# Performance work log

Hardware: AMD Instinct MI355X
Metric: run time of the kernel (lower is better)

## Reference

```python
import jax, jax.numpy as jnp
import numpy as np

B, T, D = 2, 2048, 1024
E, DFF, TOPK = 8, 4096, 2
TEMPERATURE = 1.0


def setup_inputs() -> dict:
    key = jax.random.key(0)
    k_x, k_w1, k_w2, k_r = jax.random.split(key, 4)
    x = jax.random.normal(k_x, (B, T, D), dtype=jnp.float32)
    # Expert params: linear1 [d_ff, d_model], linear2 [d_model, d_ff], stacked over experts
    W1 = jax.random.normal(k_w1, (E, DFF, D), dtype=jnp.float32) * 0.02
    W2 = jax.random.normal(k_w2, (E, D, DFF), dtype=jnp.float32) * 0.02
    Wr = jax.random.normal(k_r, (E, D), dtype=jnp.float32) * 0.02  # router linear [num_experts, d_model]
    return {"x": x, "W1": W1, "W2": W2, "Wr": Wr}


def reference(x, W1, W2, Wr):
    # ---- TemperatureRouter: softmax(logits / T) -> top-k -> renormalize ----
    logits = jnp.einsum('btd,ed->bte', x, Wr)                  # [B,T,E]
    probs = jax.nn.softmax(logits / TEMPERATURE, axis=-1)
    topk_vals, topk_idx = jax.lax.top_k(probs, TOPK)           # [B,T,K]
    router_weights = topk_vals / topk_vals.sum(-1, keepdims=True)
    # Per-token combine gate over experts (top-k indices are distinct, so this
    # matches the per-expert masked gather/scatter-add of the torch loop)
    one_hot = jax.nn.one_hot(topk_idx, E, dtype=x.dtype)       # [B,T,K,E]
    gate = jnp.einsum('btk,btke->bte', router_weights, one_hot)  # [B,T,E]
    # ---- Experts: SiLU FFN (dropout=0 / eval), dense over all experts ----
    h = jax.nn.silu(jnp.einsum('btd,efd->btef', x, W1))        # [B,T,E,DFF]
    y = jnp.einsum('btef,edf->bted', h, W2)                    # [B,T,E,D]
    out = jnp.einsum('bte,bted->btd', gate, y)                 # [B,T,D]
    return out
```

## Files before the change

### kernel.cpp

```cpp
#include <hip/hip_runtime.h>
#include <hip/hip_bf16.h>
#include <stdint.h>

#define NTOK 4096
#define DMODEL 1024
#define DFF 4096
#define NE 8
#define MAXTILE 72

typedef __attribute__((ext_vector_type(8))) short short8;
typedef __attribute__((ext_vector_type(4))) float f32x4;

__device__ inline void gload_lds16(const void* g, void* l) {
  __builtin_amdgcn_global_load_lds(
      (const __attribute__((address_space(1))) unsigned int*)g,
      (__attribute__((address_space(3))) unsigned int*)l, 16, 0, 0);
}

__global__ void k_router(const float* __restrict__ x, const float* __restrict__ Wr,
                         int* __restrict__ cnt, int* __restrict__ tok_e,
                         float* __restrict__ tok_w) {
  const int lane = threadIdx.x & 63;
  const int t = blockIdx.x * 4 + (threadIdx.x >> 6);
  float acc[NE];
#pragma unroll
  for (int e = 0; e < NE; ++e) acc[e] = 0.f;
  const float* xr = x + (size_t)t * DMODEL;
  for (int c = lane; c < DMODEL; c += 64) {
    float xv = xr[c];
#pragma unroll
    for (int e = 0; e < NE; ++e) acc[e] += xv * Wr[e * DMODEL + c];
  }
#pragma unroll
  for (int e = 0; e < NE; ++e) {
#pragma unroll
    for (int off = 32; off >= 1; off >>= 1) acc[e] += __shfl_xor(acc[e], off);
  }
  if (lane == 0) {
    int e0 = 0; float m0 = acc[0];
#pragma unroll
    for (int e = 1; e < NE; ++e) if (acc[e] > m0) { m0 = acc[e]; e0 = e; }
    int e1 = -1; float m1 = -1e30f;
#pragma unroll
    for (int e = 0; e < NE; ++e) if (e != e0 && acc[e] > m1) { m1 = acc[e]; e1 = e; }
    float w0 = 1.f / (1.f + __expf(m1 - m0));
    tok_e[2 * t] = e0; tok_e[2 * t + 1] = e1;
    tok_w[2 * t] = w0; tok_w[2 * t + 1] = 1.f - w0;
    atomicAdd(&cnt[e0], 1); atomicAdd(&cnt[e1], 1);
  }
}

__global__ void k_offsets(const int* __restrict__ cnt, int* __restrict__ cursor,
                          int* __restrict__ off, int* __restrict__ meta) {
  if (threadIdx.x == 0) {
    int s = 0;
    for (int e = 0; e < NE; ++e) { off[e] = s; cursor[e] = s; s += cnt[e]; }
    off[NE] = s;
    int nt = 0;
    for (int e = 0; e < NE; ++e)
      for (int m0 = 0; m0 < cnt[e]; m0 += 128)
        meta[1 + nt++] = (e << 16) | m0;
    meta[0] = nt;
  }
}

__global__ void k_scatter(const int* __restrict__ tok_e, const float* __restrict__ tok_w,
                          int* __restrict__ cursor, int* __restrict__ pair_token,
                          float* __restrict__ pair_w) {
  const int t = blockIdx.x * blockDim.x + threadIdx.x;
  if (t >= NTOK) return;
#pragma unroll
  for (int k = 0; k < 2; ++k) {
    int e = tok_e[2 * t + k];
    int slot = atomicAdd(&cursor[e], 1);
    pair_token[slot] = t;
    pair_w[slot] = tok_w[2 * t + k];
  }
}

__global__ void k_cvt_x(const float* __restrict__ x, __hip_bfloat16* __restrict__ xb) {
  const int i = blockIdx.x * blockDim.x + threadIdx.x;
  const float4* src = (const float4*)x + (size_t)i * 2;
  float4 v0 = src[0], v1 = src[1];
  __hip_bfloat16 o8[8];
  o8[0] = __float2bfloat16(v0.x); o8[1] = __float2bfloat16(v0.y);
  o8[2] = __float2bfloat16(v0.z); o8[3] = __float2bfloat16(v0.w);
  o8[4] = __float2bfloat16(v1.x); o8[5] = __float2bfloat16(v1.y);
  o8[6] = __float2bfloat16(v1.z); o8[7] = __float2bfloat16(v1.w);
  *reinterpret_cast<float4*>(&xb[(size_t)i * 8]) = *reinterpret_cast<float4*>(o8);
}

template <int PHASE>
__global__ __launch_bounds__(256) void k_gemm(
    const __hip_bfloat16* __restrict__ A, const float* __restrict__ Bw,
    const int* __restrict__ off, const int* __restrict__ cnt,
    const int* __restrict__ meta,
    const int* __restrict__ pair_token, const float* __restrict__ pair_w,
    __hip_bfloat16* __restrict__ h, float* __restrict__ out, int BF, int fchunk) {
  if ((int)blockIdx.y >= meta[0]) return;
  const int pk = meta[1 + blockIdx.y];
  const int e = pk >> 16;
  const int m0 = pk & 0xffff;
  const int cnt_e = cnt[e];
  const int off_e = off[e];
  const int nt = blockIdx.x;

  __shared__ __align__(16) __hip_bfloat16 Alds[128 * 64];
  __shared__ __align__(16) __hip_bfloat16 Blds[128 * 64];

  const int t = threadIdx.x;
  const int lane = t & 63;
  const int w = t >> 6, wr = w >> 1, wc = w & 1;

  const int K = (PHASE == 1) ? DMODEL : BF;
  const int Astride = (PHASE == 1) ? DMODEL : BF;
  const int Bstride = (PHASE == 1) ? DMODEL : DFF;

  const __hip_bfloat16* arow[4];
  {
    int r = t >> 3;
#pragma unroll
    for (int i = 0; i < 4; ++i) {
      int gr = m0 + r + i * 32;
      if (gr > cnt_e - 1) gr = cnt_e - 1;
      int p = off_e + gr;
      size_t row = (PHASE == 1) ? (size_t)pair_token[p] : (size_t)p;
      arow[i] = A + row * Astride;
    }
  }
  const int ac = (t & 7) * 8;

  const float* Bbase = (PHASE == 1)
      ? Bw + ((size_t)e * DFF + (size_t)fchunk * BF + (size_t)nt * 128) * DMODEL
      : Bw + ((size_t)e * DMODEL + (size_t)nt * 128) * DFF + (size_t)fchunk * BF;
  const int bl16 = t & 15;
  const int brow0 = t >> 4;

  f32x4 acc[4][4];
#pragma unroll
  for (int m = 0; m < 4; ++m)
#pragma unroll
    for (int n = 0; n < 4; ++n) acc[m][n] = (f32x4){0.f, 0.f, 0.f, 0.f};

  for (int k0 = 0; k0 < K; k0 += 64) {
    __syncthreads();
#pragma unroll
    for (int i = 0; i < 4; ++i)
      gload_lds16(arow[i] + k0 + ac, &Alds[((t >> 3) + i * 32) * 64 + ac]);
#pragma unroll
    for (int s = 0; s < 8; ++s) {
      int row = s * 16 + brow0;
      const float* bp = Bbase + (size_t)row * Bstride + k0 + bl16 * 4;
      float4 v = *(const float4*)bp;
      __hip_bfloat16 q[4];
      q[0] = __float2bfloat16(v.x); q[1] = __float2bfloat16(v.y);
      q[2] = __float2bfloat16(v.z); q[3] = __float2bfloat16(v.w);
      *(ushort4*)&Blds[row * 64 + bl16 * 4] = *(ushort4*)q;
    }
    __syncthreads();
#pragma unroll
    for (int kk = 0; kk < 2; ++kk) {
      short8 af[4], bf_[4];
      const int ko = kk * 32 + (lane >> 4) * 8;
#pragma unroll
      for (int m = 0; m < 4; ++m)
        af[m] = *(const short8*)&Alds[(wr * 64 + m * 16 + (lane & 15)) * 64 + ko];
#pragma unroll
      for (int n = 0; n < 4; ++n)
        bf_[n] = *(const short8*)&Blds[(wc * 64 + n * 16 + (lane & 15)) * 64 + ko];
#pragma unroll
      for (int m = 0; m < 4; ++m)
#pragma unroll
        for (int n = 0; n < 4; ++n)
          acc[m][n] = __builtin_amdgcn_mfma_f32_16x16x32_bf16(af[m], bf_[n], acc[m][n], 0, 0, 0);
    }
  }

#pragma unroll
  for (int m = 0; m < 4; ++m) {
#pragma unroll
    for (int j = 0; j < 4; ++j) {
      const int lrow = wr * 64 + m * 16 + (lane >> 4) * 4 + j;
      const int grow = m0 + lrow;
      if (grow >= cnt_e) continue;
      const int p = off_e + grow;
      if (PHASE == 1) {
        __hip_bfloat16* hrow = h + (size_t)p * BF;
#pragma unroll
        for (int n = 0; n < 4; ++n) {
          int col = nt * 128 + wc * 64 + n * 16 + (lane & 15);
          float v = acc[m][n][j];
          v = v / (1.f + __expf(-v));
          hrow[col] = __float2bfloat16(v);
        }
      } else {
        const int tkn = pair_token[p];
        const float wgt = pair_w[p];
        float* orow = out + (size_t)tkn * DMODEL;
#pragma unroll
        for (int n = 0; n < 4; ++n) {
          int col = nt * 128 + wc * 64 + n * 16 + (lane & 15);
          atomicAdd(&orow[col], wgt * acc[m][n][j]);
        }
      }
    }
  }
}

extern "C" void kernel_launch(void* const* d_in, const int* in_sizes, int n_in,
                              void* d_out, int out_size, void* d_ws, size_t ws_size,
                              hipStream_t stream) {
  const float* x  = (const float*)d_in[0];
  const float* W1 = (const float*)d_in[1];
  const float* W2 = (const float*)d_in[2];
  const float* Wr = (const float*)d_in[3];
  float* out = (float*)d_out;

  char* ws = (char*)d_ws;
  int*   cnt        = (int*)(ws + 0);
  int*   cursor     = (int*)(ws + 256);
  int*   off        = (int*)(ws + 512);
  int*   meta       = (int*)(ws + 768);
  int*   tok_e      = (int*)(ws + 2048);
  float* tok_w      = (float*)(ws + 2048 + 32768);
  int*   pair_token = (int*)(ws + 2048 + 65536);
  float* pair_w     = (float*)(ws + 2048 + 98304);
  __hip_bfloat16* xb = (__hip_bfloat16*)(ws + 133120);
  const size_t hoff = 133120 + (size_t)NTOK * DMODEL * 2;
  __hip_bfloat16* h = (__hip_bfloat16*)(ws + hoff);

  int nchunk = 1;
  while (nchunk < 32 &&
         hoff + (unsigned long long)(2 * NTOK) * (DFF / nchunk) * 2ULL > ws_size)
    nchunk <<= 1;
  const int BF = DFF / nchunk;

  hipMemsetAsync(cnt, 0, 32, stream);
  hipMemsetAsync(d_out, 0, (size_t)out_size * sizeof(float), stream);

  k_cvt_x<<<NTOK * DMODEL / (256 * 8), 256, 0, stream>>>(x, xb);
  k_router<<<NTOK / 4, 256, 0, stream>>>(x, Wr, cnt, tok_e, tok_w);
  k_offsets<<<1, 64, 0, stream>>>(cnt, cursor, off, meta);
  k_scatter<<<NTOK / 256, 256, 0, stream>>>(tok_e, tok_w, cursor, pair_token, pair_w);

  for (int c = 0; c < nchunk; ++c) {
    k_gemm<1><<<dim3(BF / 128, MAXTILE, 1), 256, 0, stream>>>(
        xb, W1, off, cnt, meta, pair_token, pair_w, h, out, BF, c);
    k_gemm<2><<<dim3(DMODEL / 128, MAXTILE, 1), 256, 0, stream>>>(
        h, W2, off, cnt, meta, pair_token, pair_w, h, out, BF, c);
  }
}
```

Before: 704.8 us.

## Double-buffer GEMM tiles with register prefetch and fuse x conversion into router

The expert GEMM main loop now uses two LDS buffers per operand. It prefetches the next A tile via global_load_lds and the next fp32 B tile into registers while the current tile is computed, so global memory latency overlaps with the MFMA work. The separate x-to-bf16 conversion kernel is folded into the router kernel, which already reads each token row, saving one launch and one pass over x. Launch bounds request 2 blocks per SIMD, and the doubled LDS use plus 8 float4 prefetch registers may raise register pressure or limit occupancy.

```diff
diff --git a/kernel.cpp b/kernel.cpp
--- a/kernel.cpp
+++ b/kernel.cpp
@@ -19,13 +19,27 @@
 
 __global__ void k_router(const float* __restrict__ x, const float* __restrict__ Wr,
                          int* __restrict__ cnt, int* __restrict__ tok_e,
-                         float* __restrict__ tok_w) {
+                         float* __restrict__ tok_w, __hip_bfloat16* __restrict__ xb) {
   const int lane = threadIdx.x & 63;
   const int t = blockIdx.x * 4 + (threadIdx.x >> 6);
+  const float* xr = x + (size_t)t * DMODEL;
+
+  {
+    const float4* xr4 = (const float4*)xr;
+    ushort4* xb4 = (ushort4*)(xb + (size_t)t * DMODEL);
+#pragma unroll
+    for (int i = 0; i < 4; ++i) {
+      float4 v = xr4[lane + 64 * i];
+      __hip_bfloat16 q[4];
+      q[0] = __float2bfloat16(v.x); q[1] = __float2bfloat16(v.y);
+      q[2] = __float2bfloat16(v.z); q[3] = __float2bfloat16(v.w);
+      xb4[lane + 64 * i] = *(ushort4*)q;
+    }
+  }
+
   float acc[NE];
 #pragma unroll
   for (int e = 0; e < NE; ++e) acc[e] = 0.f;
-  const float* xr = x + (size_t)t * DMODEL;
   for (int c = lane; c < DMODEL; c += 64) {
     float xv = xr[c];
 #pragma unroll
@@ -78,20 +92,8 @@
   }
 }
 
-__global__ void k_cvt_x(const float* __restrict__ x, __hip_bfloat16* __restrict__ xb) {
-  const int i = blockIdx.x * blockDim.x + threadIdx.x;
-  const float4* src = (const float4*)x + (size_t)i * 2;
-  float4 v0 = src[0], v1 = src[1];
-  __hip_bfloat16 o8[8];
-  o8[0] = __float2bfloat16(v0.x); o8[1] = __float2bfloat16(v0.y);
-  o8[2] = __float2bfloat16(v0.z); o8[3] = __float2bfloat16(v0.w);
-  o8[4] = __float2bfloat16(v1.x); o8[5] = __float2bfloat16(v1.y);
-  o8[6] = __float2bfloat16(v1.z); o8[7] = __float2bfloat16(v1.w);
-  *reinterpret_cast<float4*>(&xb[(size_t)i * 8]) = *reinterpret_cast<float4*>(o8);
-}
-
 template <int PHASE>
-__global__ __launch_bounds__(256) void k_gemm(
+__global__ __launch_bounds__(256, 2) void k_gemm(
     const __hip_bfloat16* __restrict__ A, const float* __restrict__ Bw,
     const int* __restrict__ off, const int* __restrict__ cnt,
     const int* __restrict__ meta,
@@ -105,8 +107,8 @@
   const int off_e = off[e];
   const int nt = blockIdx.x;
 
-  __shared__ __align__(16) __hip_bfloat16 Alds[128 * 64];
-  __shared__ __align__(16) __hip_bfloat16 Blds[128 * 64];
+  __shared__ __align__(16) __hip_bfloat16 Alds[2][128 * 64];
+  __shared__ __align__(16) __hip_bfloat16 Blds[2][128 * 64];
 
   const int t = threadIdx.x;
   const int lane = t & 63;
@@ -115,6 +117,7 @@
   const int K = (PHASE == 1) ? DMODEL : BF;
   const int Astride = (PHASE == 1) ? DMODEL : BF;
   const int Bstride = (PHASE == 1) ? DMODEL : DFF;
+  const int NT = K >> 6;
 
   const __hip_bfloat16* arow[4];
   {
@@ -142,38 +145,55 @@
 #pragma unroll
     for (int n = 0; n < 4; ++n) acc[m][n] = (f32x4){0.f, 0.f, 0.f, 0.f};
 
-  for (int k0 = 0; k0 < K; k0 += 64) {
-    __syncthreads();
-#pragma unroll
-    for (int i = 0; i < 4; ++i)
-      gload_lds16(arow[i] + k0 + ac, &Alds[((t >> 3) + i * 32) * 64 + ac]);
+  float4 breg[8];
+
+#pragma unroll
+  for (int i = 0; i < 4; ++i)
+    gload_lds16(arow[i] + ac, &Alds[0][((t >> 3) + i * 32) * 64 + ac]);
+#pragma unroll
+  for (int s = 0; s < 8; ++s)
+    breg[s] = *(const float4*)(Bbase + (size_t)(s * 16 + brow0) * Bstride + bl16 * 4);
+  asm volatile("s_waitcnt vmcnt(0)" ::: "memory");
+
+  for (int t_ = 0; t_ < NT; ++t_) {
+    const int cur = t_ & 1;
 #pragma unroll
     for (int s = 0; s < 8; ++s) {
       int row = s * 16 + brow0;
-      const float* bp = Bbase + (size_t)row * Bstride + k0 + bl16 * 4;
-      float4 v = *(const float4*)bp;
       __hip_bfloat16 q[4];
-      q[0] = __float2bfloat16(v.x); q[1] = __float2bfloat16(v.y);
-      q[2] = __float2bfloat16(v.z); q[3] = __float2bfloat16(v.w);
-      *(ushort4*)&Blds[row * 64 + bl16 * 4] = *(ushort4*)q;
-    }
-    __syncthreads();
+      q[0] = __float2bfloat16(breg[s].x); q[1] = __float2bfloat16(breg[s].y);
+      q[2] = __float2bfloat16(breg[s].z); q[3] = __float2bfloat16(breg[s].w);
+      *(ushort4*)&Blds[cur][row * 64 + bl16 * 4] = *(ushort4*)q;
+    }
+    if (t_ + 1 < NT) {
+      const int k0n = (t_ + 1) * 64;
+#pragma unroll
+      for (int i = 0; i < 4; ++i)
+        gload_lds16(arow[i] + k0n + ac, &Alds[cur ^ 1][((t >> 3) + i * 32) * 64 + ac]);
+#pragma unroll
+      for (int s = 0; s < 8; ++s)
+        breg[s] = *(const float4*)(Bbase + (size_t)(s * 16 + brow0) * Bstride + k0n + bl16 * 4);
+    }
+    asm volatile("s_waitcnt lgkmcnt(0)" ::: "memory");
+    __builtin_amdgcn_s_barrier();
 #pragma unroll
     for (int kk = 0; kk < 2; ++kk) {
       short8 af[4], bf_[4];
       const int ko = kk * 32 + (lane >> 4) * 8;
 #pragma unroll
       for (int m = 0; m < 4; ++m)
-        af[m] = *(const short8*)&Alds[(wr * 64 + m * 16 + (lane & 15)) * 64 + ko];
+        af[m] = *(const short8*)&Alds[cur][(wr * 64 + m * 16 + (lane & 15)) * 64 + ko];
 #pragma unroll
       for (int n = 0; n < 4; ++n)
-        bf_[n] = *(const short8*)&Blds[(wc * 64 + n * 16 + (lane & 15)) * 64 + ko];
+        bf_[n] = *(const short8*)&Blds[cur][(wc * 64 + n * 16 + (lane & 15)) * 64 + ko];
 #pragma unroll
       for (int m = 0; m < 4; ++m)
 #pragma unroll
         for (int n = 0; n < 4; ++n)
           acc[m][n] = __builtin_amdgcn_mfma_f32_16x16x32_bf16(af[m], bf_[n], acc[m][n], 0, 0, 0);
     }
+    asm volatile("s_waitcnt vmcnt(0)" ::: "memory");
+    __builtin_amdgcn_s_barrier();
   }
 
 #pragma unroll
@@ -238,8 +258,7 @@
   hipMemsetAsync(cnt, 0, 32, stream);
   hipMemsetAsync(d_out, 0, (size_t)out_size * sizeof(float), stream);
 
-  k_cvt_x<<<NTOK * DMODEL / (256 * 8), 256, 0, stream>>>(x, xb);
-  k_router<<<NTOK / 4, 256, 0, stream>>>(x, Wr, cnt, tok_e, tok_w);
+  k_router<<<NTOK / 4, 256, 0, stream>>>(x, Wr, cnt, tok_e, tok_w, xb);
   k_offsets<<<1, 64, 0, stream>>>(cnt, cursor, off, meta);
   k_scatter<<<NTOK / 256, 256, 0, stream>>>(tok_e, tok_w, cursor, pair_token, pair_w);
 
```

Measured after the change: 750.6 us. 1.06x slower.

## Pre-convert expert weights to bf16 and load B tiles via async LDS loads

Applied to the files above, without the earlier changes.

Adds a per-chunk kernel that converts the W1 and W2 chunks to bf16 once into workspace. The GEMM can then fetch B tiles with global_load_lds directly into shared memory, instead of loading fp32 through registers and converting in every tile block. The x-to-bf16 conversion is folded into the router kernel, and the GEMM gets launch_bounds occupancy hint 4. In exchange, each call pays an extra full pass over the fp32 weights (read, write bf16, re-read) and uses more workspace, which may force more chunks.

```diff
diff --git a/kernel.cpp b/kernel.cpp
--- a/kernel.cpp
+++ b/kernel.cpp
@@ -19,13 +19,27 @@
 
 __global__ void k_router(const float* __restrict__ x, const float* __restrict__ Wr,
                          int* __restrict__ cnt, int* __restrict__ tok_e,
-                         float* __restrict__ tok_w) {
+                         float* __restrict__ tok_w, __hip_bfloat16* __restrict__ xb) {
   const int lane = threadIdx.x & 63;
   const int t = blockIdx.x * 4 + (threadIdx.x >> 6);
+  const float* xr = x + (size_t)t * DMODEL;
+
+  {
+    const float4* xr4 = (const float4*)xr;
+    ushort4* xb4 = (ushort4*)(xb + (size_t)t * DMODEL);
+#pragma unroll
+    for (int i = 0; i < 4; ++i) {
+      float4 v = xr4[lane + 64 * i];
+      __hip_bfloat16 q[4];
+      q[0] = __float2bfloat16(v.x); q[1] = __float2bfloat16(v.y);
+      q[2] = __float2bfloat16(v.z); q[3] = __float2bfloat16(v.w);
+      xb4[lane + 64 * i] = *(ushort4*)q;
+    }
+  }
+
   float acc[NE];
 #pragma unroll
   for (int e = 0; e < NE; ++e) acc[e] = 0.f;
-  const float* xr = x + (size_t)t * DMODEL;
   for (int c = lane; c < DMODEL; c += 64) {
     float xv = xr[c];
 #pragma unroll
@@ -78,25 +92,28 @@
   }
 }
 
-__global__ void k_cvt_x(const float* __restrict__ x, __hip_bfloat16* __restrict__ xb) {
-  const int i = blockIdx.x * blockDim.x + threadIdx.x;
-  const float4* src = (const float4*)x + (size_t)i * 2;
-  float4 v0 = src[0], v1 = src[1];
+__global__ void k_cvt_w(const float* __restrict__ src, __hip_bfloat16* __restrict__ dst,
+                        int log2row, size_t src_stride, size_t src_coloff) {
+  const size_t i8 = ((size_t)blockIdx.x * blockDim.x + threadIdx.x) * 8;
+  const size_t row = i8 >> log2row;
+  const size_t col = i8 & (((size_t)1 << log2row) - 1);
+  const float4* s = (const float4*)(src + row * src_stride + src_coloff + col);
+  float4 v0 = s[0], v1 = s[1];
   __hip_bfloat16 o8[8];
   o8[0] = __float2bfloat16(v0.x); o8[1] = __float2bfloat16(v0.y);
   o8[2] = __float2bfloat16(v0.z); o8[3] = __float2bfloat16(v0.w);
   o8[4] = __float2bfloat16(v1.x); o8[5] = __float2bfloat16(v1.y);
   o8[6] = __float2bfloat16(v1.z); o8[7] = __float2bfloat16(v1.w);
-  *reinterpret_cast<float4*>(&xb[(size_t)i * 8]) = *reinterpret_cast<float4*>(o8);
+  *reinterpret_cast<float4*>(&dst[i8]) = *reinterpret_cast<float4*>(o8);
 }
 
 template <int PHASE>
-__global__ __launch_bounds__(256) void k_gemm(
-    const __hip_bfloat16* __restrict__ A, const float* __restrict__ Bw,
+__global__ __launch_bounds__(256, 4) void k_gemm(
+    const __hip_bfloat16* __restrict__ A, const __hip_bfloat16* __restrict__ Bw,
     const int* __restrict__ off, const int* __restrict__ cnt,
     const int* __restrict__ meta,
     const int* __restrict__ pair_token, const float* __restrict__ pair_w,
-    __hip_bfloat16* __restrict__ h, float* __restrict__ out, int BF, int fchunk) {
+    __hip_bfloat16* __restrict__ h, float* __restrict__ out, int BF) {
   if ((int)blockIdx.y >= meta[0]) return;
   const int pk = meta[1 + blockIdx.y];
   const int e = pk >> 16;
@@ -114,7 +131,7 @@
 
   const int K = (PHASE == 1) ? DMODEL : BF;
   const int Astride = (PHASE == 1) ? DMODEL : BF;
-  const int Bstride = (PHASE == 1) ? DMODEL : DFF;
+  const int Bstride = (PHASE == 1) ? DMODEL : BF;
 
   const __hip_bfloat16* arow[4];
   {
@@ -128,13 +145,17 @@
       arow[i] = A + row * Astride;
     }
   }
+  const __hip_bfloat16* Bbase = (PHASE == 1)
+      ? Bw + ((size_t)e * DFF  * 0 + (size_t)e * BF + (size_t)nt * 128) * DMODEL
+      : Bw + ((size_t)e * DMODEL + (size_t)nt * 128) * BF;
+  const __hip_bfloat16* brow[4];
+  {
+    int r = t >> 3;
+#pragma unroll
+    for (int i = 0; i < 4; ++i)
+      brow[i] = Bbase + (size_t)(r + i * 32) * Bstride;
+  }
   const int ac = (t & 7) * 8;
-
-  const float* Bbase = (PHASE == 1)
-      ? Bw + ((size_t)e * DFF + (size_t)fchunk * BF + (size_t)nt * 128) * DMODEL
-      : Bw + ((size_t)e * DMODEL + (size_t)nt * 128) * DFF + (size_t)fchunk * BF;
-  const int bl16 = t & 15;
-  const int brow0 = t >> 4;
 
   f32x4 acc[4][4];
 #pragma unroll
@@ -148,15 +169,8 @@
     for (int i = 0; i < 4; ++i)
       gload_lds16(arow[i] + k0 + ac, &Alds[((t >> 3) + i * 32) * 64 + ac]);
 #pragma unroll
-    for (int s = 0; s < 8; ++s) {
-      int row = s * 16 + brow0;
-      const float* bp = Bbase + (size_t)row * Bstride + k0 + bl16 * 4;
-      float4 v = *(const float4*)bp;
-      __hip_bfloat16 q[4];
-      q[0] = __float2bfloat16(v.x); q[1] = __float2bfloat16(v.y);
-      q[2] = __float2bfloat16(v.z); q[3] = __float2bfloat16(v.w);
-      *(ushort4*)&Blds[row * 64 + bl16 * 4] = *(ushort4*)q;
-    }
+    for (int i = 0; i < 4; ++i)
+      gload_lds16(brow[i] + k0 + ac, &Blds[((t >> 3) + i * 32) * 64 + ac]);
     __syncthreads();
 #pragma unroll
     for (int kk = 0; kk < 2; ++kk) {
@@ -226,27 +240,38 @@
   int*   pair_token = (int*)(ws + 2048 + 65536);
   float* pair_w     = (float*)(ws + 2048 + 98304);
   __hip_bfloat16* xb = (__hip_bfloat16*)(ws + 133120);
-  const size_t hoff = 133120 + (size_t)NTOK * DMODEL * 2;
-  __hip_bfloat16* h = (__hip_bfloat16*)(ws + hoff);
+  const size_t dynoff = 133120 + (size_t)NTOK * DMODEL * 2;
 
   int nchunk = 1;
   while (nchunk < 32 &&
-         hoff + (unsigned long long)(2 * NTOK) * (DFF / nchunk) * 2ULL > ws_size)
+         dynoff + 49152ULL * (DFF / nchunk) > ws_size)
     nchunk <<= 1;
   const int BF = DFF / nchunk;
 
+  __hip_bfloat16* w1b = (__hip_bfloat16*)(ws + dynoff);
+  __hip_bfloat16* w2b = w1b + (size_t)NE * BF * DMODEL;
+  __hip_bfloat16* h   = w2b + (size_t)NE * DMODEL * BF;
+
   hipMemsetAsync(cnt, 0, 32, stream);
   hipMemsetAsync(d_out, 0, (size_t)out_size * sizeof(float), stream);
 
-  k_cvt_x<<<NTOK * DMODEL / (256 * 8), 256, 0, stream>>>(x, xb);
-  k_router<<<NTOK / 4, 256, 0, stream>>>(x, Wr, cnt, tok_e, tok_w);
+  k_router<<<NTOK / 4, 256, 0, stream>>>(x, Wr, cnt, tok_e, tok_w, xb);
   k_offsets<<<1, 64, 0, stream>>>(cnt, cursor, off, meta);
   k_scatter<<<NTOK / 256, 256, 0, stream>>>(tok_e, tok_w, cursor, pair_token, pair_w);
 
+  int lg_bfdm = 0; while ((1 << lg_bfdm) < BF * DMODEL) ++lg_bfdm;
+  int lg_bf   = 0; while ((1 << lg_bf)   < BF)          ++lg_bf;
+  const int cvt_blocks = NE * BF * DMODEL / 8 / 256;
+
   for (int c = 0; c < nchunk; ++c) {
+    k_cvt_w<<<cvt_blocks, 256, 0, stream>>>(
+        W1, w1b, lg_bfdm, (size_t)DFF * DMODEL, (size_t)c * BF * DMODEL);
+    k_cvt_w<<<cvt_blocks, 256, 0, stream>>>(
+        W2, w2b, lg_bf, (size_t)DFF, (size_t)c * BF);
+
     k_gemm<1><<<dim3(BF / 128, MAXTILE, 1), 256, 0, stream>>>(
-        xb, W1, off, cnt, meta, pair_token, pair_w, h, out, BF, c);
+        xb, w1b, off, cnt, meta, pair_token, pair_w, h, out, BF);
     k_gemm<2><<<dim3(DMODEL / 128, MAXTILE, 1), 256, 0, stream>>>(
-        h, W2, off, cnt, meta, pair_token, pair_w, h, out, BF, c);
-  }
-}
+        h, w2b, off, cnt, meta, pair_token, pair_w, h, out, BF);
+  }
+}
```

Result: faster. 678.5 us (-3.7%).
